# Performance work log

Measured on AMD Instinct MI355X. Metric: run time of the kernel, lower is better.

## Reference

```python
import jax, jax.numpy as jnp
import numpy as np

LN_EPS = 1e-9
NEG_INF = float(-2**32 + 1)


def setup_inputs() -> dict:
    key = jax.random.key(0)
    k1, k2 = jax.random.split(key)
    B, T, C = 64, 1024, 256
    x = jax.random.normal(k1, (B, T, C), dtype=jnp.float32)
    key_masks = jax.random.randint(k2, (B, 1, T), 0, 2) > 0  # bool [B,1,T]
    gamma = jnp.ones((C,), dtype=jnp.float32)
    beta = jnp.zeros((C,), dtype=jnp.float32)
    return {"x": x, "key_masks": key_masks, "gamma": gamma, "beta": beta}


def reference(x, key_masks, gamma, beta):
    # x: [B,T,C]; key_masks: [B,1,T] bool; gamma/beta: [C]
    B, T, C = x.shape
    inv_scale = 1.0 / np.sqrt(C).astype(np.float32)
    # DotAttention: QK^T scaled -> [B,T,T]
    align = jnp.einsum('btc,bsc->bts', x, x) * inv_scale
    # key padding mask (broadcast over query axis)
    align = jnp.where(key_masks, align, NEG_INF)
    # future binding: causal lower-triangular mask
    causal = jnp.tril(jnp.ones((T, T), dtype=bool))
    align = jnp.where(causal[None, :, :], align, NEG_INF)
    attn = jax.nn.softmax(align, axis=-1)  # dropout_rate=0 / inference -> identity
    out = jnp.einsum('bts,bsc->btc', attn, x)  # [B,T,C]
    # LayerNorm over last axis
    mu = jnp.mean(out, axis=-1, keepdims=True)
    var = jnp.mean(jnp.square(out - mu), axis=-1, keepdims=True)
    out = gamma * (out - mu) * jax.lax.rsqrt(var + LN_EPS) + beta
    # reduce_mean over time axis, keepdims
    return jnp.mean(out, axis=1, keepdims=True)  # [B,1,C]
```

## Files before the change

kernel.cpp:

```cpp
#include <hip/hip_runtime.h>

#define B_   64
#define T_   1024
#define C_   256
#define NEGF (-4294967295.0f)
#define LN_EPS 1e-9f

typedef short  short8 __attribute__((ext_vector_type(8)));
typedef float  f32x4  __attribute__((ext_vector_type(4)));

union S8 { short8 v; unsigned int w[4]; };

__device__ __forceinline__ unsigned int pk2(float x, float y) {
  unsigned a = __float_as_uint(x); a = (a + 0x7fffu + ((a >> 16) & 1u)) >> 16;
  unsigned b = __float_as_uint(y); b = (b + 0x7fffu + ((b >> 16) & 1u)) >> 16;
  return a | (b << 16);
}

__device__ __forceinline__ void async16(const void* g, void* l) {
  __builtin_amdgcn_global_load_lds(
      (const __attribute__((address_space(1))) void*)g,
      (__attribute__((address_space(3))) void*)l,
      16, 0, 0);
}


__global__ void detect_kernel(const unsigned int* __restrict__ mw,
                              int* __restrict__ flag) {
  int idx = blockIdx.x * 256 + threadIdx.x;
  if (mw[idx] > 1u) atomicOr(flag, 1);
}

__global__ void finalize_kernel(const float* __restrict__ accum,
                                float* __restrict__ out) {
  int idx = blockIdx.x * 256 + threadIdx.x;
  out[idx] = accum[idx] * (1.0f / T_);
}

__global__ __launch_bounds__(256) void convert2(const float* __restrict__ x,
                                                const unsigned int* __restrict__ mw,
                                                const int* __restrict__ flag,
                                                short* __restrict__ xk,
                                                short* __restrict__ xv,
                                                float* __restrict__ colsum,
                                                float2* __restrict__ sb) {
  const int blk = blockIdx.x;
  const int b   = blk >> 3, e8 = blk & 7;
  const int tid = threadIdx.x;
  const float* xb = x + (size_t)b * (T_ * C_);

  if (tid < 128) {
    int idx = b * 1024 + e8 * 128 + tid;
    int f = *flag;
    unsigned int w = mw[f ? (idx >> 2) : idx];
    unsigned int v = f ? ((w >> ((idx & 3) * 8)) & 0xffu) : w;
    sb[idx] = v ? make_float2(0.0625f, 0.f) : make_float2(0.f, NEGF);
  }

  float cacc = 0.f;

  for (int st = 0; st < 4; ++st) {
    const int tt = e8 * 4 + st;
    const float* xt = xb + (size_t)tt * 32 * 256;

#pragma unroll
    for (int u = 0; u < 4; ++u) {
      int id = u * 256 + tid;
      int row = id >> 5, ck = id & 31;
      const float* src = xt + row * 256 + ck * 8;
      float4 a  = *(const float4*)src;
      float4 c4 = *(const float4*)(src + 4);
      S8 s; s.w[0] = pk2(a.x, a.y);  s.w[1] = pk2(a.z, a.w);
            s.w[2] = pk2(c4.x, c4.y); s.w[3] = pk2(c4.z, c4.w);
      *(short8*)(xk + (size_t)(b * 1024 + tt * 32 + row) * 256 + ((ck ^ row) << 3)) = s.v;
    }

    const int c = tid;
    short* vout = xv + (size_t)(b * 32 + tt) * 8192;
#pragma unroll
    for (int jc = 0; jc < 4; ++jc) {
      float vs[8];
#pragma unroll
      for (int ee = 0; ee < 8; ++ee) {
        vs[ee] = xt[(jc * 8 + ee) * 256 + c];
        cacc += vs[ee];
      }
      S8 o;
      o.w[0] = pk2(vs[0], vs[1]); o.w[1] = pk2(vs[2], vs[3]);
      o.w[2] = pk2(vs[4], vs[5]); o.w[3] = pk2(vs[6], vs[7]);
      *(short8*)(vout + c * 32 + (((jc ^ ((c >> 1) & 3)) & 3) << 3)) = o.v;
    }
  }
  atomicAdd(&colsum[b * 256 + tid], cacc);
}

__device__ __forceinline__ void finalize_tile(
    f32x4* Oa, float m, float l, int b, int quad, int r,
    const float* __restrict__ colsum, const float* __restrict__ gamma,
    const float* __restrict__ beta, float* __restrict__ accum)
{
  float mr[4], li[4];
#pragma unroll
  for (int reg = 0; reg < 4; ++reg) {
    mr[reg] = __shfl(m, quad * 4 + reg, 64);
    float lr = __shfl(l, quad * 4 + reg, 64);
    li[reg] = 1.f / lr;
  }
#pragma unroll
  for (int ct = 0; ct < 16; ++ct) {
    float cs = colsum[b * C_ + ct * 16 + r] * (1.0f / T_);
#pragma unroll
    for (int reg = 0; reg < 4; ++reg)
      Oa[ct][reg] = (mr[reg] < -1.0e9f) ? cs : Oa[ct][reg] * li[reg];
  }
  float ts[16];
#pragma unroll
  for (int ct = 0; ct < 16; ++ct) ts[ct] = 0.f;
#pragma unroll
  for (int reg = 0; reg < 4; ++reg) {
    float s2 = 0.f;
#pragma unroll
    for (int ct = 0; ct < 16; ++ct) s2 += Oa[ct][reg];
    s2 += __shfl_xor(s2, 1, 64); s2 += __shfl_xor(s2, 2, 64);
    s2 += __shfl_xor(s2, 4, 64); s2 += __shfl_xor(s2, 8, 64);
    float mu = s2 * (1.0f / C_);
    float sq = 0.f;
#pragma unroll
    for (int ct = 0; ct < 16; ++ct) { float d = Oa[ct][reg] - mu; sq += d * d; }
    sq += __shfl_xor(sq, 1, 64); sq += __shfl_xor(sq, 2, 64);
    sq += __shfl_xor(sq, 4, 64); sq += __shfl_xor(sq, 8, 64);
    float rstd = rsqrtf(sq * (1.0f / C_) + LN_EPS);
#pragma unroll
    for (int ct = 0; ct < 16; ++ct) {
      int c = ct * 16 + r;
      ts[ct] += gamma[c] * (Oa[ct][reg] - mu) * rstd + beta[c];
    }
  }
#pragma unroll
  for (int ct = 0; ct < 16; ++ct) {
    ts[ct] += __shfl_xor(ts[ct], 16, 64);
    ts[ct] += __shfl_xor(ts[ct], 32, 64);
  }
  if (quad == 0) {
#pragma unroll
    for (int ct = 0; ct < 16; ++ct)
      atomicAdd(&accum[b * C_ + ct * 16 + r], ts[ct]);
  }
}

__global__ __launch_bounds__(512, 2) void flash5(
    const short* __restrict__ xk,
    const short* __restrict__ xv,
    const float2* __restrict__ sb,
    const float* __restrict__ gamma,
    const float* __restrict__ beta,
    const float* __restrict__ colsum,
    float* __restrict__ accum)
{
  __shared__ __align__(16) short KsD[2][64 * 256];
  __shared__ __align__(16) short VtD[2][2 * 256 * 32];

  const int i0 = blockIdx.x;
  const int x8 = i0 & 7;
  const int s  = i0 >> 3;
  const int b  = x8 + 8 * (s & 7);
  const int t  = s >> 3;

  const int tid  = threadIdx.x;
  const int w    = tid >> 6;
  const int lane = tid & 63;
  const int quad = lane >> 4;
  const int r    = lane & 15;

  const int h0len = 2 * (t + 1);

  int qt   = t;
  int n0   = qt * 128 + w * 16;
  int qrow = n0 + r;
  short8 qf[8];
  {
    const short* qp = xk + (size_t)(b * 1024 + qrow) * 256;
#pragma unroll
    for (int ks = 0; ks < 8; ++ks)
      qf[ks] = *(const short8*)(qp + (((ks * 4 + quad) ^ (qrow & 31)) << 3));
  }
  f32x4 Oa[16];
#pragma unroll
  for (int ct = 0; ct < 16; ++ct) Oa[ct] = (f32x4){0.f, 0.f, 0.f, 0.f};
  float m = NEGF, l = 0.f;

  {
    const short* gk = xk + (size_t)(b * 1024) * 256;
    const short* gv = xv + (size_t)(b * 32) * 8192;
#pragma unroll
    for (int u = 0; u < 4; ++u) {
      int seg = w * 4 + u;
      async16(gk + seg * 512 + lane * 8, &KsD[0][seg * 512]);
      async16(gv + seg * 512 + lane * 8, &VtD[0][seg * 512]);
    }
  }
  __syncthreads();

  for (int idx = 0; idx < 18; ++idx) {
    const int ibuf = idx & 1;
    if (idx < 17) {
      const int nt2 = (idx + 1 < h0len) ? (idx + 1) : (17 - (idx + 1));
      const short* gk = xk + (size_t)(b * 1024 + nt2 * 64) * 256;
      const short* gv = xv + (size_t)(b * 32 + nt2 * 2) * 8192;
#pragma unroll
      for (int u = 0; u < 4; ++u) {
        int seg = w * 4 + u;
        async16(gk + seg * 512 + lane * 8, &KsD[1 - ibuf][seg * 512]);
        async16(gv + seg * 512 + lane * 8, &VtD[1 - ibuf][seg * 512]);
      }
    }

    const int kt  = (idx < h0len) ? idx : (17 - idx);
    const int ktb = kt * 64;
    if (ktb <= n0 + 15) {
      float sc[16];
#pragma unroll
      for (int mt = 0; mt < 4; ++mt) {
        f32x4 acc = (f32x4){0.f, 0.f, 0.f, 0.f};
        const int row = mt * 16 + r;
#pragma unroll
        for (int ks = 0; ks < 8; ++ks) {
          short8 af = *(short8*)&KsD[ibuf][row * 256 + (((ks * 4 + quad) ^ (row & 31)) << 3)];
          acc = __builtin_amdgcn_mfma_f32_16x16x32_bf16(af, qf[ks], acc, 0, 0, 0);
        }
        const int j0 = ktb + mt * 16 + quad * 4;
        float4 sA = *(const float4*)(sb + (size_t)b * 1024 + j0);
        float4 sB = *(const float4*)(sb + (size_t)b * 1024 + j0 + 2);
        sc[mt * 4 + 0] = acc[0] * sA.x + sA.y;
        sc[mt * 4 + 1] = acc[1] * sA.z + sA.w;
        sc[mt * 4 + 2] = acc[2] * sB.x + sB.y;
        sc[mt * 4 + 3] = acc[3] * sB.z + sB.w;
      }
      if (ktb + 63 > n0) {
#pragma unroll
        for (int k2 = 0; k2 < 16; ++k2) {
          int j = ktb + (k2 >> 2) * 16 + quad * 4 + (k2 & 3);
          if (j > qrow) sc[k2] = NEGF;
        }
      }

      float mx = sc[0];
#pragma unroll
      for (int k2 = 1; k2 < 16; ++k2) mx = fmaxf(mx, sc[k2]);
      mx = fmaxf(mx, __shfl_xor(mx, 16, 64));
      mx = fmaxf(mx, __shfl_xor(mx, 32, 64));
      float mnew  = fmaxf(m, mx);
      float alpha = __expf(m - mnew);
      float p[16], ps = 0.f;
#pragma unroll
      for (int k2 = 0; k2 < 16; ++k2) { p[k2] = __expf(sc[k2] - mnew); ps += p[k2]; }
      ps += __shfl_xor(ps, 16, 64);
      ps += __shfl_xor(ps, 32, 64);
      l = l * alpha + ps;
      m = mnew;

      if (__ballot(alpha < 1.0f)) {
        float ar[4];
#pragma unroll
        for (int reg = 0; reg < 4; ++reg) ar[reg] = __shfl(alpha, quad * 4 + reg, 64);
#pragma unroll
        for (int ct = 0; ct < 16; ++ct) {
          Oa[ct][0] *= ar[0]; Oa[ct][1] *= ar[1];
          Oa[ct][2] *= ar[2]; Oa[ct][3] *= ar[3];
        }
      }

      S8 pf[2];
#pragma unroll
      for (int hh = 0; hh < 2; ++hh) {
        unsigned q0 = pk2(p[hh * 8 + 0], p[hh * 8 + 1]);
        unsigned q1 = pk2(p[hh * 8 + 2], p[hh * 8 + 3]);
        unsigned q2 = pk2(p[hh * 8 + 4], p[hh * 8 + 5]);
        unsigned q3 = pk2(p[hh * 8 + 6], p[hh * 8 + 7]);
        int s0l = ((quad & 1) << 5) + r, s1l = s0l + 16;
        unsigned u0 = __shfl((int)q0, s0l, 64), u1 = __shfl((int)q1, s0l, 64);
        unsigned u2 = __shfl((int)q2, s0l, 64), u3 = __shfl((int)q3, s0l, 64);
        unsigned v0 = __shfl((int)q0, s1l, 64), v1 = __shfl((int)q1, s1l, 64);
        unsigned v2 = __shfl((int)q2, s1l, 64), v3 = __shfl((int)q3, s1l, 64);
        bool hi = quad >= 2;
        pf[hh].w[0] = hi ? u2 : u0; pf[hh].w[1] = hi ? u3 : u1;
        pf[hh].w[2] = hi ? v2 : v0; pf[hh].w[3] = hi ? v3 : v1;
      }

#pragma unroll
      for (int ct = 0; ct < 16; ++ct) {
        int c = ct * 16 + r;
        int cs_off = c * 32 + (((quad ^ ((c >> 1) & 3)) & 3) << 3);
        short8 b0 = *(short8*)&VtD[ibuf][cs_off];
        short8 b1 = *(short8*)&VtD[ibuf][8192 + cs_off];
        Oa[ct] = __builtin_amdgcn_mfma_f32_16x16x32_bf16(pf[0].v, b0, Oa[ct], 0, 0, 0);
        Oa[ct] = __builtin_amdgcn_mfma_f32_16x16x32_bf16(pf[1].v, b1, Oa[ct], 0, 0, 0);
      }
    }

    if (idx == h0len - 1) {
      finalize_tile(Oa, m, l, b, quad, r, colsum, gamma, beta, accum);
      qt = 7 - t;
      n0 = qt * 128 + w * 16;
      qrow = n0 + r;
      const short* qp = xk + (size_t)(b * 1024 + qrow) * 256;
#pragma unroll
      for (int ks = 0; ks < 8; ++ks)
        qf[ks] = *(const short8*)(qp + (((ks * 4 + quad) ^ (qrow & 31)) << 3));
#pragma unroll
      for (int ct = 0; ct < 16; ++ct) Oa[ct] = (f32x4){0.f, 0.f, 0.f, 0.f};
      m = NEGF; l = 0.f;
    }

    __syncthreads();
  }

  finalize_tile(Oa, m, l, b, quad, r, colsum, gamma, beta, accum);
}


extern "C" void kernel_launch(void* const* d_in, const int* in_sizes, int n_in,
                              void* d_out, int out_size, void* d_ws, size_t ws_size,
                              hipStream_t stream) {
  const float* x     = (const float*)d_in[0];
  const void*  km    = d_in[1];
  const float* gamma = (const float*)d_in[2];
  const float* beta  = (const float*)d_in[3];
  float* out = (float*)d_out;

  const size_t off_sb = 131200;
  const size_t off_xk = 655616;
  const size_t off_xv = off_xk + 33554432;

  float*  accum  = (float*)d_ws;
  float*  colsum = (float*)((char*)d_ws + 65536);
  int*    flag   = (int*)((char*)d_ws + 131072);
  float2* sb     = (float2*)((char*)d_ws + off_sb);
  short*  xk     = (short*)((char*)d_ws + off_xk);
  short*  xv     = (short*)((char*)d_ws + off_xv);

  hipMemsetAsync(d_ws, 0, 131136, stream);
  detect_kernel<<<64, 256, 0, stream>>>((const unsigned int*)km, flag);
  convert2<<<512, 256, 0, stream>>>(x, (const unsigned int*)km, flag,
                                    xk, xv, colsum, sb);
  flash5<<<256, 512, 0, stream>>>(xk, xv, sb, gamma, beta, colsum, accum);
  finalize_kernel<<<B_ * C_ / 256, 256, 0, stream>>>(accum, out);
}
```

Before: 188.9 us.

## Fuse conversion and mask detection into flash kernel with inter-block flags

Merges the mask-format detection, bf16 conversion/transpose, column-sum and finalize kernels into the single attention kernel. Each block converts its own quarter of one batch, staging rows in LDS to build the transposed V layout, then publishes per-quarter ready flags that other blocks spin-wait on before loading those tiles. A global grid-wide counter barrier follows mask detection. This removes separate launches and the accumulator pass, at the cost of relying on all 256 blocks being co-resident and on spin-wait synchronisation. The V tile layout is also changed to a rotation-based swizzle.

```diff
diff --git a/kernel.cpp b/kernel.cpp
--- a/kernel.cpp
+++ b/kernel.cpp
@@ -5,6 +5,7 @@
 #define C_   256
 #define NEGF (-4294967295.0f)
 #define LN_EPS 1e-9f
+#define XSTR 268
 
 typedef short  short8 __attribute__((ext_vector_type(8)));
 typedef float  f32x4  __attribute__((ext_vector_type(4)));
@@ -24,80 +25,10 @@
       16, 0, 0);
 }
 
-
-__global__ void detect_kernel(const unsigned int* __restrict__ mw,
-                              int* __restrict__ flag) {
-  int idx = blockIdx.x * 256 + threadIdx.x;
-  if (mw[idx] > 1u) atomicOr(flag, 1);
-}
-
-__global__ void finalize_kernel(const float* __restrict__ accum,
-                                float* __restrict__ out) {
-  int idx = blockIdx.x * 256 + threadIdx.x;
-  out[idx] = accum[idx] * (1.0f / T_);
-}
-
-__global__ __launch_bounds__(256) void convert2(const float* __restrict__ x,
-                                                const unsigned int* __restrict__ mw,
-                                                const int* __restrict__ flag,
-                                                short* __restrict__ xk,
-                                                short* __restrict__ xv,
-                                                float* __restrict__ colsum,
-                                                float2* __restrict__ sb) {
-  const int blk = blockIdx.x;
-  const int b   = blk >> 3, e8 = blk & 7;
-  const int tid = threadIdx.x;
-  const float* xb = x + (size_t)b * (T_ * C_);
-
-  if (tid < 128) {
-    int idx = b * 1024 + e8 * 128 + tid;
-    int f = *flag;
-    unsigned int w = mw[f ? (idx >> 2) : idx];
-    unsigned int v = f ? ((w >> ((idx & 3) * 8)) & 0xffu) : w;
-    sb[idx] = v ? make_float2(0.0625f, 0.f) : make_float2(0.f, NEGF);
-  }
-
-  float cacc = 0.f;
-
-  for (int st = 0; st < 4; ++st) {
-    const int tt = e8 * 4 + st;
-    const float* xt = xb + (size_t)tt * 32 * 256;
-
-#pragma unroll
-    for (int u = 0; u < 4; ++u) {
-      int id = u * 256 + tid;
-      int row = id >> 5, ck = id & 31;
-      const float* src = xt + row * 256 + ck * 8;
-      float4 a  = *(const float4*)src;
-      float4 c4 = *(const float4*)(src + 4);
-      S8 s; s.w[0] = pk2(a.x, a.y);  s.w[1] = pk2(a.z, a.w);
-            s.w[2] = pk2(c4.x, c4.y); s.w[3] = pk2(c4.z, c4.w);
-      *(short8*)(xk + (size_t)(b * 1024 + tt * 32 + row) * 256 + ((ck ^ row) << 3)) = s.v;
-    }
-
-    const int c = tid;
-    short* vout = xv + (size_t)(b * 32 + tt) * 8192;
-#pragma unroll
-    for (int jc = 0; jc < 4; ++jc) {
-      float vs[8];
-#pragma unroll
-      for (int ee = 0; ee < 8; ++ee) {
-        vs[ee] = xt[(jc * 8 + ee) * 256 + c];
-        cacc += vs[ee];
-      }
-      S8 o;
-      o.w[0] = pk2(vs[0], vs[1]); o.w[1] = pk2(vs[2], vs[3]);
-      o.w[2] = pk2(vs[4], vs[5]); o.w[3] = pk2(vs[6], vs[7]);
-      *(short8*)(vout + c * 32 + (((jc ^ ((c >> 1) & 3)) & 3) << 3)) = o.v;
-    }
-  }
-  atomicAdd(&colsum[b * 256 + tid], cacc);
-}
-
 __device__ __forceinline__ void finalize_tile(
     f32x4* Oa, float m, float l, int b, int quad, int r,
     const float* __restrict__ colsum, const float* __restrict__ gamma,
-    const float* __restrict__ beta, float* __restrict__ accum)
+    const float* __restrict__ beta, float* __restrict__ out)
 {
   float mr[4], li[4];
 #pragma unroll
@@ -144,21 +75,28 @@
   if (quad == 0) {
 #pragma unroll
     for (int ct = 0; ct < 16; ++ct)
-      atomicAdd(&accum[b * C_ + ct * 16 + r], ts[ct]);
-  }
-}
-
-__global__ __launch_bounds__(512, 2) void flash5(
-    const short* __restrict__ xk,
-    const short* __restrict__ xv,
-    const float2* __restrict__ sb,
+      atomicAdd(&out[b * C_ + ct * 16 + r], ts[ct] * (1.0f / T_));
+  }
+}
+
+__global__ __launch_bounds__(512, 2) void flash6(
+    const float* __restrict__ x,
+    const unsigned int* __restrict__ mw,
     const float* __restrict__ gamma,
     const float* __restrict__ beta,
-    const float* __restrict__ colsum,
-    float* __restrict__ accum)
+    float* __restrict__ out,
+    short* __restrict__ xk,
+    short* __restrict__ xv,
+    float2* __restrict__ sb,
+    float* __restrict__ colsum,
+    int* __restrict__ dflag,
+    int* __restrict__ scanDone,
+    int* __restrict__ qflags)
 {
-  __shared__ __align__(16) short KsD[2][64 * 256];
-  __shared__ __align__(16) short VtD[2][2 * 256 * 32];
+  __shared__ __align__(16) char smem[131072];
+  short (*KsD)[64 * 256] = (short (*)[64 * 256])smem;
+  short (*VtD)[2 * 8192] = (short (*)[2 * 8192])(smem + 65536);
+  float* Xt = (float*)smem;
 
   const int i0 = blockIdx.x;
   const int x8 = i0 & 7;
@@ -172,12 +110,88 @@
   const int quad = lane >> 4;
   const int r    = lane & 15;
 
+  if (tid < 64) {
+    unsigned int v = mw[i0 * 64 + tid];
+    unsigned long long bl = __ballot(v > 1u);
+    if (tid == 0 && bl) atomicOr(dflag, 1);
+  }
+  __syncthreads();
+  if (tid == 0) {
+    __threadfence();
+    atomicAdd(scanDone, 1);
+    while (__hip_atomic_load(scanDone, __ATOMIC_ACQUIRE, __HIP_MEMORY_SCOPE_AGENT) < 256)
+      __builtin_amdgcn_s_sleep(2);
+  }
+  __syncthreads();
+  const int df = __hip_atomic_load(dflag, __ATOMIC_RELAXED, __HIP_MEMORY_SCOPE_AGENT);
+
+  const float* xb = x + (size_t)b * (T_ * C_);
+  short* xkb = xk + (size_t)(b * 1024) * 256;
+  float cpart = 0.f;
+  const int ccol = tid & 255, chalf = tid >> 8;
+
+  for (int sub = 0; sub < 4; ++sub) {
+    const int r0 = t * 256 + sub * 64;
+#pragma unroll
+    for (int u = 0; u < 4; ++u) {
+      int id = u * 512 + tid, row = id >> 5, ck = id & 31;
+      const float* src = xb + (size_t)(r0 + row) * 256 + ck * 8;
+      float4 a  = *(const float4*)src;
+      float4 c4 = *(const float4*)(src + 4);
+      *(float4*)&Xt[row * XSTR + ck * 8]     = a;
+      *(float4*)&Xt[row * XSTR + ck * 8 + 4] = c4;
+      S8 sv; sv.w[0] = pk2(a.x, a.y);  sv.w[1] = pk2(a.z, a.w);
+             sv.w[2] = pk2(c4.x, c4.y); sv.w[3] = pk2(c4.z, c4.w);
+      *(short8*)(xkb + (size_t)(r0 + row) * 256 + ((ck ^ ((r0 + row) & 31)) << 3)) = sv.v;
+    }
+    __syncthreads();
+#pragma unroll
+    for (int pass = 0; pass < 4; ++pass) {
+      int aG = pass * 512 + tid;
+      int tileL = aG >> 10, a = aG & 1023;
+      int q = a >> 8, c = ((a & 255) - (q << 2)) & 255;
+      int jb = tileL * 32 + q * 8;
+      float vs[8];
+#pragma unroll
+      for (int e = 0; e < 8; ++e) vs[e] = Xt[(jb + e) * XSTR + c];
+      S8 o;
+      o.w[0] = pk2(vs[0], vs[1]); o.w[1] = pk2(vs[2], vs[3]);
+      o.w[2] = pk2(vs[4], vs[5]); o.w[3] = pk2(vs[6], vs[7]);
+      *(short8*)(xv + (size_t)(b * 32 + t * 8 + sub * 2 + tileL) * 8192 + (aG & 1023) * 8) = o.v;
+    }
+#pragma unroll
+    for (int e = 0; e < 32; ++e) cpart += Xt[(chalf * 32 + e) * XSTR + ccol];
+    __syncthreads();
+  }
+  atomicAdd(&colsum[b * C_ + ccol], cpart);
+  if (tid < 256) {
+    int idx = b * 1024 + t * 256 + tid;
+    unsigned int wv = mw[df ? (idx >> 2) : idx];
+    unsigned int v = df ? ((wv >> ((idx & 3) * 8)) & 0xffu) : wv;
+    sb[idx] = v ? make_float2(0.0625f, 0.f) : make_float2(0.f, NEGF);
+  }
+  __syncthreads();
+  if (tid == 0) {
+    __threadfence();
+    __hip_atomic_store(&qflags[b * 4 + t], 1, __ATOMIC_RELEASE, __HIP_MEMORY_SCOPE_AGENT);
+  }
+
+  unsigned seen = 1u << t;
+#define GATE(q)                                                                     \
+  if (!(seen & (1u << (q)))) {                                                      \
+    while (__hip_atomic_load(&qflags[b * 4 + (q)], __ATOMIC_ACQUIRE,                \
+                             __HIP_MEMORY_SCOPE_AGENT) == 0)                        \
+      __builtin_amdgcn_s_sleep(2);                                                  \
+    seen |= 1u << (q);                                                              \
+  }
+
   const int h0len = 2 * (t + 1);
 
   int qt   = t;
   int n0   = qt * 128 + w * 16;
   int qrow = n0 + r;
   short8 qf[8];
+  GATE(t >> 1);
   {
     const short* qp = xk + (size_t)(b * 1024 + qrow) * 256;
 #pragma unroll
@@ -189,6 +203,7 @@
   for (int ct = 0; ct < 16; ++ct) Oa[ct] = (f32x4){0.f, 0.f, 0.f, 0.f};
   float m = NEGF, l = 0.f;
 
+  GATE(0);
   {
     const short* gk = xk + (size_t)(b * 1024) * 256;
     const short* gv = xv + (size_t)(b * 32) * 8192;
@@ -205,6 +220,7 @@
     const int ibuf = idx & 1;
     if (idx < 17) {
       const int nt2 = (idx + 1 < h0len) ? (idx + 1) : (17 - (idx + 1));
+      GATE(nt2 >> 2);
       const short* gk = xk + (size_t)(b * 1024 + nt2 * 64) * 256;
       const short* gv = xv + (size_t)(b * 32 + nt2 * 2) * 8192;
 #pragma unroll
@@ -290,19 +306,21 @@
 #pragma unroll
       for (int ct = 0; ct < 16; ++ct) {
         int c = ct * 16 + r;
-        int cs_off = c * 32 + (((quad ^ ((c >> 1) & 3)) & 3) << 3);
-        short8 b0 = *(short8*)&VtD[ibuf][cs_off];
-        short8 b1 = *(short8*)&VtD[ibuf][8192 + cs_off];
+        int a0 = (quad << 8) + ((c + (quad << 2)) & 255);
+        short8 b0 = *(short8*)&VtD[ibuf][a0 << 3];
+        short8 b1 = *(short8*)&VtD[ibuf][8192 + (a0 << 3)];
         Oa[ct] = __builtin_amdgcn_mfma_f32_16x16x32_bf16(pf[0].v, b0, Oa[ct], 0, 0, 0);
         Oa[ct] = __builtin_amdgcn_mfma_f32_16x16x32_bf16(pf[1].v, b1, Oa[ct], 0, 0, 0);
       }
     }
 
     if (idx == h0len - 1) {
-      finalize_tile(Oa, m, l, b, quad, r, colsum, gamma, beta, accum);
+      GATE(0); GATE(1); GATE(2); GATE(3);
+      finalize_tile(Oa, m, l, b, quad, r, colsum, gamma, beta, out);
       qt = 7 - t;
       n0 = qt * 128 + w * 16;
       qrow = n0 + r;
+      GATE(qt >> 1);
       const short* qp = xk + (size_t)(b * 1024 + qrow) * 256;
 #pragma unroll
       for (int ks = 0; ks < 8; ++ks)
@@ -315,7 +333,8 @@
     __syncthreads();
   }
 
-  finalize_tile(Oa, m, l, b, quad, r, colsum, gamma, beta, accum);
+  finalize_tile(Oa, m, l, b, quad, r, colsum, gamma, beta, out);
+#undef GATE
 }
 
 
@@ -332,17 +351,16 @@
   const size_t off_xk = 655616;
   const size_t off_xv = off_xk + 33554432;
 
-  float*  accum  = (float*)d_ws;
-  float*  colsum = (float*)((char*)d_ws + 65536);
-  int*    flag   = (int*)((char*)d_ws + 131072);
-  float2* sb     = (float2*)((char*)d_ws + off_sb);
-  short*  xk     = (short*)((char*)d_ws + off_xk);
-  short*  xv     = (short*)((char*)d_ws + off_xv);
-
-  hipMemsetAsync(d_ws, 0, 131136, stream);
-  detect_kernel<<<64, 256, 0, stream>>>((const unsigned int*)km, flag);
-  convert2<<<512, 256, 0, stream>>>(x, (const unsigned int*)km, flag,
-                                    xk, xv, colsum, sb);
-  flash5<<<256, 512, 0, stream>>>(xk, xv, sb, gamma, beta, colsum, accum);
-  finalize_kernel<<<B_ * C_ / 256, 256, 0, stream>>>(accum, out);
-}
+  float*  colsum   = (float*)d_ws;
+  int*    dflag    = (int*)((char*)d_ws + 65536);
+  int*    scanDone = (int*)((char*)d_ws + 65540);
+  int*    qflags   = (int*)((char*)d_ws + 65544);
+  float2* sb       = (float2*)((char*)d_ws + off_sb);
+  short*  xk       = (short*)((char*)d_ws + off_xk);
+  short*  xv       = (short*)((char*)d_ws + off_xv);
+
+  hipMemsetAsync(d_ws, 0, 66568, stream);
+  hipMemsetAsync(d_out, 0, 65536, stream);
+  flash6<<<256, 512, 0, stream>>>(x, (const unsigned int*)km, gamma, beta, out,
+                                  xk, xv, sb, colsum, dflag, scanDone, qflags);
+}
```

Result: slower. 241.6 us (+27.9%).
